# Kernel optimization log

Measured on AMD Instinct MI355X. Metric: run time of the kernel, lower is better.

The kernel has to match this reference:

```python
import jax, jax.numpy as jnp
import numpy as np

N = 100000   # nodes
E = 1600000  # edges (avg degree 16)
D = 128      # in_features == out_features (required by residual branch)


def setup_inputs() -> dict:
    key = jax.random.key(0)
    ks = jax.random.split(key, 8)
    return {
        "x": jax.random.normal(ks[0], (N, D), dtype=jnp.float32),
        "W": jax.random.normal(ks[1], (D, D), dtype=jnp.float32) * (1.0 / np.sqrt(D)),
        "b": jax.random.normal(ks[2], (D,), dtype=jnp.float32) * 0.01,
        "Wres": jax.random.normal(ks[3], (D, D), dtype=jnp.float32) * (1.0 / np.sqrt(D)),
        "bres": jax.random.normal(ks[4], (D,), dtype=jnp.float32) * 0.01,
        "edge_val": jax.random.uniform(ks[5], (E,), dtype=jnp.float32),
        "edge_row": jax.random.randint(ks[6], (E,), 0, N, dtype=jnp.int32),
        "edge_col": jax.random.randint(ks[7], (E,), 0, N, dtype=jnp.int32),
    }


def reference(x, W, b, Wres, bres, edge_val, edge_row, edge_col):
    # Dense projection: [N, D]
    h = x @ W + b
    # Sparse adjacency SpMM: out[i] = sum_{e: row[e]==i} val[e] * h[col[e]]
    msgs = edge_val[:, None] * h[edge_col]            # [E, D] gather
    agg = jax.ops.segment_sum(msgs, edge_row, num_segments=N)  # [N, D] scatter-add
    # Activation (relu), then residual Linear applied to post-activation tensor
    # (faithful to the torch code: x = act(x); x = x + residual(x)).
    a = jax.nn.relu(agg)
    out = a + (a @ Wres + bres)
    # dropout = 0.0 -> identity (eval mode)
    return out
```

## Files before the change

kernel.cpp:

```cpp
#include <hip/hip_runtime.h>
#include <hip/hip_bf16.h>

#define D 128
#define RCH 128
#define NCH 782
#define NCHP 1024
#define NB_S 500
#define CH_S 3200
#define OS2 800
#define CAP 3072
#define PB 128

typedef __attribute__((ext_vector_type(8))) short short8v;
typedef __attribute__((ext_vector_type(4))) float float4v;

__device__ inline ushort f2bf(float f) {
    __hip_bfloat16 h = __float2bfloat16(f);
    return __builtin_bit_cast(ushort, h);
}
__device__ inline float bf2f(ushort u) {
    return __builtin_bit_cast(float, (uint)u << 16);
}
__device__ inline ushort relu_bf(ushort u) { return (u & 0x8000u) ? (ushort)0 : u; }

__device__ inline void stage_wt_lds(char* smem, const ushort* __restrict__ Wt,
                                    int tid) {
#pragma unroll
    for (int i = 0; i < 8; ++i) {
        const int L = tid * 128 + i * 16;
        const int row = L >> 8;
        const int off = L & 255;
        *(short8v*)(smem + row * 256 + (off ^ ((row & 7) << 4))) =
            *(const short8v*)((const char*)Wt + L);
    }
}

__global__ __launch_bounds__(256) void k1_prep(const float* __restrict__ W,
                                               const float* __restrict__ Wres,
                                               ushort* __restrict__ Wt,
                                               ushort* __restrict__ Wtres) {
    const int flat = blockIdx.x * 256 + threadIdx.x;
    const float* src = (flat < 16384) ? W : Wres;
    ushort* dst = (flat < 16384) ? Wt : Wtres;
    const int f = flat & 16383;
    const int k = f >> 7, c = f & 127;
    dst[c * D + k] = f2bf(src[f]);
}

__global__ __launch_bounds__(256) void k3a_scatter(const float* __restrict__ ev,
                                                   const int* __restrict__ er,
                                                   const int* __restrict__ ec,
                                                   int* __restrict__ offs2,
                                                   int2* __restrict__ tmp, int E) {
    __shared__ int h[NCHP];
    __shared__ int sscan[256];
    const int b = blockIdx.x;
    const int t = threadIdx.x;
    const int start = b * CH_S;
    const int end = min(E, start + CH_S);
    const int nfull = (end - start) & ~3;

    for (int k = t; k < NCHP; k += 256) h[k] = 0;
    __syncthreads();

    for (int o = 4 * t; o < nfull; o += 1024) {
        const int4 r4 = *(const int4*)(er + start + o);
        atomicAdd(&h[r4.x >> 7], 1);
        atomicAdd(&h[r4.y >> 7], 1);
        atomicAdd(&h[r4.z >> 7], 1);
        atomicAdd(&h[r4.w >> 7], 1);
    }
    for (int o = nfull + t; o < end - start; o += 256)
        atomicAdd(&h[er[start + o] >> 7], 1);
    __syncthreads();

    const int a0 = h[4 * t], a1 = h[4 * t + 1];
    const int a2 = h[4 * t + 2], a3 = h[4 * t + 3];
    const int tsum = a0 + a1 + a2 + a3;
    sscan[t] = tsum;
    __syncthreads();
    for (int o = 1; o < 256; o <<= 1) {
        const int a = (t >= o) ? sscan[t - o] : 0;
        __syncthreads();
        sscan[t] += a;
        __syncthreads();
    }
    const int ex = start + sscan[t] - tsum;
    const int c0 = 4 * t;
    h[c0]     = ex;
    h[c0 + 1] = ex + a0;
    h[c0 + 2] = ex + a0 + a1;
    h[c0 + 3] = ex + a0 + a1 + a2;
    int* od = offs2 + (long)b * OS2;
#pragma unroll
    for (int i = 0; i < 4; ++i)
        if (c0 + i <= NCH) od[c0 + i] = h[c0 + i];
    __syncthreads();

    for (int o = 4 * t; o < nfull; o += 1024) {
        const int4 r4 = *(const int4*)(er + start + o);
        const int4 c4 = *(const int4*)(ec + start + o);
        const float4 v4 = *(const float4*)(ev + start + o);
        const int p0 = atomicAdd(&h[r4.x >> 7], 1);
        const int p1 = atomicAdd(&h[r4.y >> 7], 1);
        const int p2 = atomicAdd(&h[r4.z >> 7], 1);
        const int p3 = atomicAdd(&h[r4.w >> 7], 1);
        tmp[p0] = make_int2((c4.x << 7) | (r4.x & 127), __float_as_int(v4.x));
        tmp[p1] = make_int2((c4.y << 7) | (r4.y & 127), __float_as_int(v4.y));
        tmp[p2] = make_int2((c4.z << 7) | (r4.z & 127), __float_as_int(v4.z));
        tmp[p3] = make_int2((c4.w << 7) | (r4.w & 127), __float_as_int(v4.w));
    }
    for (int o = nfull + t; o < end - start; o += 256) {
        const int e = start + o;
        const int r = er[e];
        const int pos = atomicAdd(&h[r >> 7], 1);
        tmp[pos] = make_int2((ec[e] << 7) | (r & 127), __float_as_int(ev[e]));
    }
}

__global__ __launch_bounds__(256) void k3b_gemm0(const float* __restrict__ X,
                                                 const ushort* __restrict__ Wt,
                                                 const float* __restrict__ bias,
                                                 ushort* __restrict__ hb, int N) {
    __shared__ char smem[32768];
    const int lane = threadIdx.x & 63;
    const int w = threadIdx.x >> 6;
    const int l16 = lane & 15;
    const int lk = lane >> 4;

    stage_wt_lds(smem, Wt, threadIdx.x);
    __syncthreads();

    const int swz = (l16 & 7) << 4;

#pragma unroll
    for (int j = 0; j < 2; ++j) {
        const long wRow = (long)blockIdx.x * 128 + j * 64 + w * 16;

        short8v afrag[4];
        {
            long r = wRow + l16;
            if (r >= N) r = N - 1;
            const float* xp = X + r * D + lk * 8;
#pragma unroll
            for (int ks = 0; ks < 4; ++ks) {
                const float4 u0 = *(const float4*)(xp + ks * 32);
                const float4 u1 = *(const float4*)(xp + ks * 32 + 4);
                float f[8] = {u0.x, u0.y, u0.z, u0.w, u1.x, u1.y, u1.z, u1.w};
                short8v a;
#pragma unroll
                for (int i = 0; i < 8; ++i) a[i] = (short)f2bf(f[i]);
                afrag[ks] = a;
            }
        }

        float4v acc[8];
#pragma unroll
        for (int t = 0; t < 8; ++t) acc[t] = (float4v)(0.0f);

#pragma unroll
        for (int ks = 0; ks < 4; ++ks) {
#pragma unroll
            for (int t = 0; t < 8; ++t) {
                const int row = t * 16 + l16;
                const short8v bfrag = *(const short8v*)(
                    smem + row * 256 + ((ks * 64 + lk * 16) ^ swz));
                acc[t] = __builtin_amdgcn_mfma_f32_16x16x32_bf16(afrag[ks], bfrag,
                                                                 acc[t], 0, 0, 0);
            }
        }

#pragma unroll
        for (int t = 0; t < 8; ++t) {
            const int col = t * 16 + l16;
            const float bb = bias[col];
#pragma unroll
            for (int i = 0; i < 4; ++i) {
                const long row = wRow + lk * 4 + i;
                if (row < N) hb[row * D + col] = f2bf(acc[t][i] + bb);
            }
        }
    }
}

__global__ __launch_bounds__(256) void k4_sort(const int2* __restrict__ tmp,
                                               const int* __restrict__ offs2,
                                               int2* __restrict__ recs,
                                               int* __restrict__ rowptr) {
    __shared__ int2 buf[CAP];
    __shared__ int sb[256];
    __shared__ int hcnt[RCH];
    __shared__ int sc[RCH];
    __shared__ int cur[RCH];
    const int c = blockIdx.x;
    const int t = threadIdx.x;
    const int s = c * CAP;

    int segA = 0, cbA = 0, segB = 0, cbB = 0;
    if (t < NB_S / 2) {
        const int* oA = offs2 + (long)(2 * t) * OS2;
        const int* oB = offs2 + (long)(2 * t + 1) * OS2;
        segA = oA[c]; cbA = oA[c + 1] - segA;
        segB = oB[c]; cbB = oB[c + 1] - segB;
    }
    const int cb = cbA + cbB;

    sb[t] = cb;
    __syncthreads();
    for (int o = 1; o < 256; o <<= 1) {
        const int a = (t >= o) ? sb[t - o] : 0;
        __syncthreads();
        sb[t] += a;
        __syncthreads();
    }
    const int base = sb[t] - cb;
    const int cnt = min(sb[255], CAP);

    if (t < RCH) hcnt[t] = 0;
    __syncthreads();

    for (int i = 0; i < cbA; ++i) {
        const int p = base + i;
        if (p >= CAP) break;
        const int2 r = tmp[segA + i];
        buf[p] = r;
        atomicAdd(&hcnt[r.x & 127], 1);
    }
    for (int i = 0; i < cbB; ++i) {
        const int p = base + cbA + i;
        if (p >= CAP) break;
        const int2 r = tmp[segB + i];
        buf[p] = r;
        atomicAdd(&hcnt[r.x & 127], 1);
    }
    __syncthreads();

    if (t < RCH) sc[t] = hcnt[t];
    __syncthreads();
    for (int o = 1; o < RCH; o <<= 1) {
        const int a = (t < RCH && t >= o) ? sc[t - o] : 0;
        __syncthreads();
        if (t < RCH) sc[t] += a;
        __syncthreads();
    }
    if (t < RCH) {
        const int ex = s + sc[t] - hcnt[t];
        cur[t] = ex;
        rowptr[c * (RCH + 1) + t] = ex;
    }
    if (t == 0) rowptr[c * (RCH + 1) + RCH] = s + cnt;
    __syncthreads();

    for (int k = t; k < cnt; k += 256) {
        const int2 r = buf[k];
        const int pos = atomicAdd(&cur[r.x & 127], 1);
        recs[pos] = make_int2((r.x >> 7) << 8, r.y);
    }
}

#define GFMA2(accv, rr, gg)                                                   \
    accv.x = fmaf(__int_as_float((rr).y), bf2f((ushort)((gg)&0xffffu)), accv.x);\
    accv.y = fmaf(__int_as_float((rr).y), bf2f((ushort)((gg) >> 16)), accv.y);

__device__ inline void drain_row(const int2* __restrict__ recs,
                                 const char* __restrict__ hpc,
                                 int& j, int e, float2& acc) {
    for (; j + 8 <= e; j += 8) {
        const int2 r0 = recs[j],     r1 = recs[j + 1];
        const int2 r2 = recs[j + 2], r3 = recs[j + 3];
        const int2 r4 = recs[j + 4], r5 = recs[j + 5];
        const int2 r6 = recs[j + 6], r7 = recs[j + 7];
        const uint g0 = *(const uint*)(hpc + (uint)r0.x);
        const uint g1 = *(const uint*)(hpc + (uint)r1.x);
        const uint g2 = *(const uint*)(hpc + (uint)r2.x);
        const uint g3 = *(const uint*)(hpc + (uint)r3.x);
        const uint g4 = *(const uint*)(hpc + (uint)r4.x);
        const uint g5 = *(const uint*)(hpc + (uint)r5.x);
        const uint g6 = *(const uint*)(hpc + (uint)r6.x);
        const uint g7 = *(const uint*)(hpc + (uint)r7.x);
        GFMA2(acc, r0, g0) GFMA2(acc, r1, g1) GFMA2(acc, r2, g2) GFMA2(acc, r3, g3)
        GFMA2(acc, r4, g4) GFMA2(acc, r5, g5) GFMA2(acc, r6, g6) GFMA2(acc, r7, g7)
    }
    for (; j + 2 <= e; j += 2) {
        const int2 r0 = recs[j], r1 = recs[j + 1];
        const uint g0 = *(const uint*)(hpc + (uint)r0.x);
        const uint g1 = *(const uint*)(hpc + (uint)r1.x);
        GFMA2(acc, r0, g0) GFMA2(acc, r1, g1)
    }
    if (j < e) {
        const int2 r0 = recs[j];
        const uint g0 = *(const uint*)(hpc + (uint)r0.x);
        GFMA2(acc, r0, g0)
    }
}

__global__ __launch_bounds__(256) void k5_spmm(const ushort* __restrict__ hb,
                                               const int2* __restrict__ recs,
                                               const int* __restrict__ rowptr,
                                               ushort* __restrict__ aggb, int N) {
    const int pair = blockIdx.x * 4 + (threadIdx.x >> 6);
    const int lane = threadIdx.x & 63;
    const int rowA = pair * 2;
    if (rowA >= N) return;

    const int c = rowA >> 7;
    const int tr = rowA & 127;
    int rp = 0;
    if (lane < 3) rp = rowptr[c * (RCH + 1) + tr + lane];
    const int sA = __shfl(rp, 0);
    const int eA = __shfl(rp, 1);
    const int sB = eA;
    const int eB = __shfl(rp, 2);

    const char* hpc = (const char*)hb + lane * 4;
    float2 accA = make_float2(0.f, 0.f);
    float2 accB = make_float2(0.f, 0.f);

    int jA = sA, jB = sB;
    while (jA + 8 <= eA && jB + 8 <= eB) {
        const int2 a0 = recs[jA],     a1 = recs[jA + 1];
        const int2 a2 = recs[jA + 2], a3 = recs[jA + 3];
        const int2 a4 = recs[jA + 4], a5 = recs[jA + 5];
        const int2 a6 = recs[jA + 6], a7 = recs[jA + 7];
        const int2 b0 = recs[jB],     b1 = recs[jB + 1];
        const int2 b2 = recs[jB + 2], b3 = recs[jB + 3];
        const int2 b4 = recs[jB + 4], b5 = recs[jB + 5];
        const int2 b6 = recs[jB + 6], b7 = recs[jB + 7];
        const uint ga0 = *(const uint*)(hpc + (uint)a0.x);
        const uint ga1 = *(const uint*)(hpc + (uint)a1.x);
        const uint ga2 = *(const uint*)(hpc + (uint)a2.x);
        const uint ga3 = *(const uint*)(hpc + (uint)a3.x);
        const uint ga4 = *(const uint*)(hpc + (uint)a4.x);
        const uint ga5 = *(const uint*)(hpc + (uint)a5.x);
        const uint ga6 = *(const uint*)(hpc + (uint)a6.x);
        const uint ga7 = *(const uint*)(hpc + (uint)a7.x);
        const uint gb0 = *(const uint*)(hpc + (uint)b0.x);
        const uint gb1 = *(const uint*)(hpc + (uint)b1.x);
        const uint gb2 = *(const uint*)(hpc + (uint)b2.x);
        const uint gb3 = *(const uint*)(hpc + (uint)b3.x);
        const uint gb4 = *(const uint*)(hpc + (uint)b4.x);
        const uint gb5 = *(const uint*)(hpc + (uint)b5.x);
        const uint gb6 = *(const uint*)(hpc + (uint)b6.x);
        const uint gb7 = *(const uint*)(hpc + (uint)b7.x);
        GFMA2(accA, a0, ga0) GFMA2(accA, a1, ga1) GFMA2(accA, a2, ga2) GFMA2(accA, a3, ga3)
        GFMA2(accA, a4, ga4) GFMA2(accA, a5, ga5) GFMA2(accA, a6, ga6) GFMA2(accA, a7, ga7)
        GFMA2(accB, b0, gb0) GFMA2(accB, b1, gb1) GFMA2(accB, b2, gb2) GFMA2(accB, b3, gb3)
        GFMA2(accB, b4, gb4) GFMA2(accB, b5, gb5) GFMA2(accB, b6, gb6) GFMA2(accB, b7, gb7)
        jA += 8;
        jB += 8;
    }
    drain_row(recs, hpc, jA, eA, accA);
    drain_row(recs, hpc, jB, eB, accB);

    const uint pA = (uint)f2bf(accA.x) | ((uint)f2bf(accA.y) << 16);
    *(uint*)(aggb + (long)rowA * D + lane * 2) = pA;
    const uint pB = (uint)f2bf(accB.x) | ((uint)f2bf(accB.y) << 16);
    *(uint*)(aggb + (long)(rowA + 1) * D + lane * 2) = pB;
}

__global__ __launch_bounds__(256) void k6_gemm1(const ushort* __restrict__ Xb,
                                                const ushort* __restrict__ Wt,
                                                const float* __restrict__ bias,
                                                float* __restrict__ Y, int N) {
    __shared__ char smem[32768];
    const int lane = threadIdx.x & 63;
    const int w = threadIdx.x >> 6;
    const int l16 = lane & 15;
    const int lk = lane >> 4;
    const long wRow = (long)blockIdx.x * 64 + w * 16;

    short8v afrag[4];
    {
        long r = wRow + l16;
        if (r >= N) r = N - 1;
        const ushort* xp = Xb + r * D + lk * 8;
#pragma unroll
        for (int ks = 0; ks < 4; ++ks) {
            short8v a = *(const short8v*)(xp + ks * 32);
#pragma unroll
            for (int i = 0; i < 8; ++i) a[i] = (short)relu_bf((ushort)a[i]);
            afrag[ks] = a;
        }
    }

    stage_wt_lds(smem, Wt, threadIdx.x);
    __syncthreads();

    float4v acc[8];
#pragma unroll
    for (int t = 0; t < 8; ++t) acc[t] = (float4v)(0.0f);

    const int swz = (l16 & 7) << 4;
#pragma unroll
    for (int ks = 0; ks < 4; ++ks) {
#pragma unroll
        for (int t = 0; t < 8; ++t) {
            const int row = t * 16 + l16;
            const short8v bfrag = *(const short8v*)(
                smem + row * 256 + ((ks * 64 + lk * 16) ^ swz));
            acc[t] = __builtin_amdgcn_mfma_f32_16x16x32_bf16(afrag[ks], bfrag,
                                                             acc[t], 0, 0, 0);
        }
    }

#pragma unroll
    for (int t = 0; t < 8; ++t) {
        const int col = t * 16 + l16;
        const float bb = bias[col];
#pragma unroll
        for (int i = 0; i < 4; ++i) {
            const long row = wRow + lk * 4 + i;
            if (row < N) {
                const float a = bf2f(relu_bf(Xb[row * D + col]));
                Y[row * D + col] = a + acc[t][i] + bb;
            }
        }
    }
}

extern "C" void kernel_launch(void* const* d_in, const int* in_sizes, int n_in,
                              void* d_out, int out_size, void* d_ws, size_t ws_size,
                              hipStream_t stream) {
    const float* x    = (const float*)d_in[0];
    const float* W    = (const float*)d_in[1];
    const float* b    = (const float*)d_in[2];
    const float* Wres = (const float*)d_in[3];
    const float* bres = (const float*)d_in[4];
    const float* ev   = (const float*)d_in[5];
    const int*   er   = (const int*)d_in[6];
    const int*   ec   = (const int*)d_in[7];

    float* out = (float*)d_out;

    const int n = in_sizes[0] / D;
    const int e = in_sizes[5];

    char* ws = (char*)d_ws;
    size_t off_b = 0;
    auto alloc = [&](size_t bytes) {
        void* p = ws + off_b;
        off_b += (bytes + 511) & ~size_t(511);
        return p;
    };
    ushort* hb     = (ushort*)alloc((size_t)n * D * sizeof(ushort));
    int2*   recs   = (int2*)alloc((size_t)NCH * CAP * sizeof(int2));
    int*    rowptr = (int*)alloc((size_t)NCH * (RCH + 1) * sizeof(int));
    ushort* Wt     = (ushort*)alloc((size_t)D * D * sizeof(ushort));
    ushort* Wtres  = (ushort*)alloc((size_t)D * D * sizeof(ushort));
    const size_t overlay = off_b;
    int2*   tmp    = (int2*)alloc((size_t)NB_S * CH_S * sizeof(int2));
    int*    offs2  = (int*)alloc((size_t)NB_S * OS2 * sizeof(int));
    size_t aggb_end = overlay + (size_t)n * D * sizeof(ushort);
    if (aggb_end > off_b) off_b = aggb_end;
    ushort* aggb = (ushort*)(ws + overlay);
    (void)ws_size;

    k1_prep<<<PB, 256, 0, stream>>>(W, Wres, Wt, Wtres);

    k3a_scatter<<<NB_S, 256, 0, stream>>>(ev, er, ec, offs2, tmp, e);

    k3b_gemm0<<<(n + 127) / 128, 256, 0, stream>>>(x, Wt, b, hb, n);

    k4_sort<<<NCH, 256, 0, stream>>>(tmp, offs2, recs, rowptr);

    k5_spmm<<<(n / 2 + 3) / 4, 256, 0, stream>>>(hb, recs, rowptr, aggb, n);

    k6_gemm1<<<(n + 63) / 64, 256, 0, stream>>>(aggb, Wtres, bres, out, n);
}
```

Baseline: 162.4 us.

## Band-sort edges by source column and process four rows per wave in SpMM

The per-chunk counting sort now uses 2048 buckets keyed by destination row plus a high-bit band of the column byte offset, so each row's edges are ordered by column band. The aim is better L2/cache locality for the h gathers across waves running at the same time. The SpMM kernel also processes four rows per wavefront instead of two, with 32 independent gathers in flight to raise memory-level parallelism. The costs are a larger LDS footprint and a longer prefix scan in the sort, plus higher register pressure in the SpMM, which may lower occupancy.

```diff
diff --git a/kernel.cpp b/kernel.cpp
--- a/kernel.cpp
+++ b/kernel.cpp
@@ -10,6 +10,8 @@
 #define OS2 800
 #define CAP 3072
 #define PB 128
+#define NBKT 2048
+#define BANDSH 20
 
 typedef __attribute__((ext_vector_type(8))) short short8v;
 typedef __attribute__((ext_vector_type(4))) float float4v;
@@ -189,9 +191,8 @@
                                                int* __restrict__ rowptr) {
     __shared__ int2 buf[CAP];
     __shared__ int sb[256];
-    __shared__ int hcnt[RCH];
-    __shared__ int sc[RCH];
-    __shared__ int cur[RCH];
+    __shared__ int bcnt[NBKT];
+    __shared__ int bcur[NBKT];
     const int c = blockIdx.x;
     const int t = threadIdx.x;
     const int s = c * CAP;
@@ -206,6 +207,7 @@
     const int cb = cbA + cbB;
 
     sb[t] = cb;
+    for (int k = t; k < NBKT; k += 256) bcnt[k] = 0;
     __syncthreads();
     for (int o = 1; o < 256; o <<= 1) {
         const int a = (t >= o) ? sb[t - o] : 0;
@@ -216,44 +218,45 @@
     const int base = sb[t] - cb;
     const int cnt = min(sb[255], CAP);
 
-    if (t < RCH) hcnt[t] = 0;
-    __syncthreads();
-
     for (int i = 0; i < cbA; ++i) {
         const int p = base + i;
         if (p >= CAP) break;
         const int2 r = tmp[segA + i];
         buf[p] = r;
-        atomicAdd(&hcnt[r.x & 127], 1);
+        atomicAdd(&bcnt[((r.x & 127) << 4) | (r.x >> BANDSH)], 1);
     }
     for (int i = 0; i < cbB; ++i) {
         const int p = base + cbA + i;
         if (p >= CAP) break;
         const int2 r = tmp[segB + i];
         buf[p] = r;
-        atomicAdd(&hcnt[r.x & 127], 1);
-    }
-    __syncthreads();
-
-    if (t < RCH) sc[t] = hcnt[t];
-    __syncthreads();
-    for (int o = 1; o < RCH; o <<= 1) {
-        const int a = (t < RCH && t >= o) ? sc[t - o] : 0;
+        atomicAdd(&bcnt[((r.x & 127) << 4) | (r.x >> BANDSH)], 1);
+    }
+    __syncthreads();
+
+    int v[8];
+    int tsum = 0;
+#pragma unroll
+    for (int i = 0; i < 8; ++i) { v[i] = bcnt[8 * t + i]; tsum += v[i]; }
+    sb[t] = tsum;
+    __syncthreads();
+    for (int o = 1; o < 256; o <<= 1) {
+        const int a = (t >= o) ? sb[t - o] : 0;
         __syncthreads();
-        if (t < RCH) sc[t] += a;
+        sb[t] += a;
         __syncthreads();
     }
-    if (t < RCH) {
-        const int ex = s + sc[t] - hcnt[t];
-        cur[t] = ex;
-        rowptr[c * (RCH + 1) + t] = ex;
-    }
+    int run = s + sb[t] - tsum;
+#pragma unroll
+    for (int i = 0; i < 8; ++i) { bcur[8 * t + i] = run; run += v[i]; }
+    __syncthreads();
+    if (t < RCH) rowptr[c * (RCH + 1) + t] = bcur[t << 4];
     if (t == 0) rowptr[c * (RCH + 1) + RCH] = s + cnt;
     __syncthreads();
 
     for (int k = t; k < cnt; k += 256) {
         const int2 r = buf[k];
-        const int pos = atomicAdd(&cur[r.x & 127], 1);
+        const int pos = atomicAdd(&bcur[((r.x & 127) << 4) | (r.x >> BANDSH)], 1);
         recs[pos] = make_int2((r.x >> 7) << 8, r.y);
     }
 }
@@ -294,29 +297,10 @@
     }
 }
 
-__global__ __launch_bounds__(256) void k5_spmm(const ushort* __restrict__ hb,
-                                               const int2* __restrict__ recs,
-                                               const int* __restrict__ rowptr,
-                                               ushort* __restrict__ aggb, int N) {
-    const int pair = blockIdx.x * 4 + (threadIdx.x >> 6);
-    const int lane = threadIdx.x & 63;
-    const int rowA = pair * 2;
-    if (rowA >= N) return;
-
-    const int c = rowA >> 7;
-    const int tr = rowA & 127;
-    int rp = 0;
-    if (lane < 3) rp = rowptr[c * (RCH + 1) + tr + lane];
-    const int sA = __shfl(rp, 0);
-    const int eA = __shfl(rp, 1);
-    const int sB = eA;
-    const int eB = __shfl(rp, 2);
-
-    const char* hpc = (const char*)hb + lane * 4;
-    float2 accA = make_float2(0.f, 0.f);
-    float2 accB = make_float2(0.f, 0.f);
-
-    int jA = sA, jB = sB;
+__device__ inline void pair_loop(const int2* __restrict__ recs,
+                                 const char* __restrict__ hpc,
+                                 int& jA, int eA, int& jB, int eB,
+                                 float2& accA, float2& accB) {
     while (jA + 8 <= eA && jB + 8 <= eB) {
         const int2 a0 = recs[jA],     a1 = recs[jA + 1];
         const int2 a2 = recs[jA + 2], a3 = recs[jA + 3];
@@ -349,13 +333,68 @@
         jA += 8;
         jB += 8;
     }
-    drain_row(recs, hpc, jA, eA, accA);
-    drain_row(recs, hpc, jB, eB, accB);
-
-    const uint pA = (uint)f2bf(accA.x) | ((uint)f2bf(accA.y) << 16);
-    *(uint*)(aggb + (long)rowA * D + lane * 2) = pA;
-    const uint pB = (uint)f2bf(accB.x) | ((uint)f2bf(accB.y) << 16);
-    *(uint*)(aggb + (long)(rowA + 1) * D + lane * 2) = pB;
+}
+
+__global__ __launch_bounds__(256) void k5_spmm(const ushort* __restrict__ hb,
+                                               const int2* __restrict__ recs,
+                                               const int* __restrict__ rowptr,
+                                               ushort* __restrict__ aggb, int N) {
+    const int quad = blockIdx.x * 4 + (threadIdx.x >> 6);
+    const int lane = threadIdx.x & 63;
+    const int row0 = quad * 4;
+    if (row0 >= N) return;
+
+    const int c = row0 >> 7;
+    const int tr = row0 & 127;
+    int rp = 0;
+    if (lane < 5) rp = rowptr[c * (RCH + 1) + tr + lane];
+    int js[4], es[4];
+    js[0] = __shfl(rp, 0); es[0] = __shfl(rp, 1);
+    js[1] = es[0];         es[1] = __shfl(rp, 2);
+    js[2] = es[1];         es[2] = __shfl(rp, 3);
+    js[3] = es[2];         es[3] = __shfl(rp, 4);
+
+    const char* hpc = (const char*)hb + lane * 4;
+    float2 ac[4];
+#pragma unroll
+    for (int s = 0; s < 4; ++s) ac[s] = make_float2(0.f, 0.f);
+
+    while (js[0] + 8 <= es[0] && js[1] + 8 <= es[1] &&
+           js[2] + 8 <= es[2] && js[3] + 8 <= es[3]) {
+        int2 r[4][8];
+        uint g[4][8];
+#pragma unroll
+        for (int s = 0; s < 4; ++s) {
+#pragma unroll
+            for (int i = 0; i < 8; ++i) r[s][i] = recs[js[s] + i];
+        }
+#pragma unroll
+        for (int s = 0; s < 4; ++s) {
+#pragma unroll
+            for (int i = 0; i < 8; ++i)
+                g[s][i] = *(const uint*)(hpc + (uint)r[s][i].x);
+        }
+#pragma unroll
+        for (int s = 0; s < 4; ++s) {
+#pragma unroll
+            for (int i = 0; i < 8; ++i) { GFMA2(ac[s], r[s][i], g[s][i]) }
+            js[s] += 8;
+        }
+    }
+
+    pair_loop(recs, hpc, js[0], es[0], js[1], es[1], ac[0], ac[1]);
+    pair_loop(recs, hpc, js[2], es[2], js[3], es[3], ac[2], ac[3]);
+
+    drain_row(recs, hpc, js[0], es[0], ac[0]);
+    drain_row(recs, hpc, js[1], es[1], ac[1]);
+    drain_row(recs, hpc, js[2], es[2], ac[2]);
+    drain_row(recs, hpc, js[3], es[3], ac[3]);
+
+#pragma unroll
+    for (int s = 0; s < 4; ++s) {
+        const uint p = (uint)f2bf(ac[s].x) | ((uint)f2bf(ac[s].y) << 16);
+        *(uint*)(aggb + (long)(row0 + s) * D + lane * 2) = p;
+    }
 }
 
 __global__ __launch_bounds__(256) void k6_gemm1(const ushort* __restrict__ Xb,
@@ -463,7 +502,7 @@
 
     k4_sort<<<NCH, 256, 0, stream>>>(tmp, offs2, recs, rowptr);
 
-    k5_spmm<<<(n / 2 + 3) / 4, 256, 0, stream>>>(hb, recs, rowptr, aggb, n);
+    k5_spmm<<<(n / 4 + 3) / 4, 256, 0, stream>>>(hb, recs, rowptr, aggb, n);
 
     k6_gemm1<<<(n + 63) / 64, 256, 0, stream>>>(aggb, Wtres, bres, out, n);
 }
```

Result: slower. 175.7 us (+8.2%).

## Merge independent kernels into heterogeneous launches to cut launch count

Applied to the files above, without the earlier changes.

Folds the weight-transpose prep blocks into the edge scatter kernel and the bucket sort blocks into the first GEMM kernel, selecting the role by block index. This takes the launch count from six to four and lets independent work share one grid. The GEMM part now handles 64 rows per block instead of 128, so twice as many blocks each restage the weights into LDS. The sort's shared buffers are carved out of the GEMM's 32 KB shared array, so both roles get the same LDS footprint.

```diff
diff --git a/kernel.cpp b/kernel.cpp
--- a/kernel.cpp
+++ b/kernel.cpp
@@ -10,6 +10,7 @@
 #define OS2 800
 #define CAP 3072
 #define PB 128
+#define GB64 1563
 
 typedef __attribute__((ext_vector_type(8))) short short8v;
 typedef __attribute__((ext_vector_type(4))) float float4v;
@@ -35,25 +36,25 @@
     }
 }
 
-__global__ __launch_bounds__(256) void k1_prep(const float* __restrict__ W,
-                                               const float* __restrict__ Wres,
-                                               ushort* __restrict__ Wt,
-                                               ushort* __restrict__ Wtres) {
-    const int flat = blockIdx.x * 256 + threadIdx.x;
-    const float* src = (flat < 16384) ? W : Wres;
-    ushort* dst = (flat < 16384) ? Wt : Wtres;
-    const int f = flat & 16383;
-    const int k = f >> 7, c = f & 127;
-    dst[c * D + k] = f2bf(src[f]);
-}
-
-__global__ __launch_bounds__(256) void k3a_scatter(const float* __restrict__ ev,
-                                                   const int* __restrict__ er,
-                                                   const int* __restrict__ ec,
-                                                   int* __restrict__ offs2,
-                                                   int2* __restrict__ tmp, int E) {
+__global__ __launch_bounds__(256) void kA_scatter_prep(
+    const float* __restrict__ W, const float* __restrict__ Wres,
+    ushort* __restrict__ Wt, ushort* __restrict__ Wtres,
+    const float* __restrict__ ev, const int* __restrict__ er,
+    const int* __restrict__ ec, int* __restrict__ offs2,
+    int2* __restrict__ tmp, int E) {
     __shared__ int h[NCHP];
     __shared__ int sscan[256];
+
+    if (blockIdx.x >= NB_S) {
+        const int flat = (blockIdx.x - NB_S) * 256 + threadIdx.x;
+        const float* src = (flat < 16384) ? W : Wres;
+        ushort* dst = (flat < 16384) ? Wt : Wtres;
+        const int f = flat & 16383;
+        const int k = f >> 7, c = f & 127;
+        dst[c * D + k] = f2bf(src[f]);
+        return;
+    }
+
     const int b = blockIdx.x;
     const int t = threadIdx.x;
     const int start = b * CH_S;
@@ -118,143 +119,139 @@
     }
 }
 
-__global__ __launch_bounds__(256) void k3b_gemm0(const float* __restrict__ X,
-                                                 const ushort* __restrict__ Wt,
-                                                 const float* __restrict__ bias,
-                                                 ushort* __restrict__ hb, int N) {
+__global__ __launch_bounds__(256) void kB_sort_gemm(
+    const int2* __restrict__ tmp, const int* __restrict__ offs2,
+    int2* __restrict__ recs, int* __restrict__ rowptr,
+    const float* __restrict__ X, const ushort* __restrict__ Wt,
+    const float* __restrict__ bias, ushort* __restrict__ hb, int N) {
     __shared__ char smem[32768];
-    const int lane = threadIdx.x & 63;
-    const int w = threadIdx.x >> 6;
+    const int t = threadIdx.x;
+
+    if (blockIdx.x < NCH) {
+        int2* buf = (int2*)smem;
+        int*  sb  = (int*)(smem + 24576);
+        int*  hcnt = (int*)(smem + 25600);
+        int*  sc  = (int*)(smem + 26112);
+        int*  cur = (int*)(smem + 26624);
+        const int c = blockIdx.x;
+        const int s = c * CAP;
+
+        int segA = 0, cbA = 0, segB = 0, cbB = 0;
+        if (t < NB_S / 2) {
+            const int* oA = offs2 + (long)(2 * t) * OS2;
+            const int* oB = offs2 + (long)(2 * t + 1) * OS2;
+            segA = oA[c]; cbA = oA[c + 1] - segA;
+            segB = oB[c]; cbB = oB[c + 1] - segB;
+        }
+        const int cb = cbA + cbB;
+
+        sb[t] = cb;
+        __syncthreads();
+        for (int o = 1; o < 256; o <<= 1) {
+            const int a = (t >= o) ? sb[t - o] : 0;
+            __syncthreads();
+            sb[t] += a;
+            __syncthreads();
+        }
+        const int base = sb[t] - cb;
+        const int cnt = min(sb[255], CAP);
+
+        if (t < RCH) hcnt[t] = 0;
+        __syncthreads();
+
+        for (int i = 0; i < cbA; ++i) {
+            const int p = base + i;
+            if (p >= CAP) break;
+            const int2 r = tmp[segA + i];
+            buf[p] = r;
+            atomicAdd(&hcnt[r.x & 127], 1);
+        }
+        for (int i = 0; i < cbB; ++i) {
+            const int p = base + cbA + i;
+            if (p >= CAP) break;
+            const int2 r = tmp[segB + i];
+            buf[p] = r;
+            atomicAdd(&hcnt[r.x & 127], 1);
+        }
+        __syncthreads();
+
+        if (t < RCH) sc[t] = hcnt[t];
+        __syncthreads();
+        for (int o = 1; o < RCH; o <<= 1) {
+            const int a = (t < RCH && t >= o) ? sc[t - o] : 0;
+            __syncthreads();
+            if (t < RCH) sc[t] += a;
+            __syncthreads();
+        }
+        if (t < RCH) {
+            const int ex = s + sc[t] - hcnt[t];
+            cur[t] = ex;
+            rowptr[c * (RCH + 1) + t] = ex;
+        }
+        if (t == 0) rowptr[c * (RCH + 1) + RCH] = s + cnt;
+        __syncthreads();
+
+        for (int k = t; k < cnt; k += 256) {
+            const int2 r = buf[k];
+            const int pos = atomicAdd(&cur[r.x & 127], 1);
+            recs[pos] = make_int2((r.x >> 7) << 8, r.y);
+        }
+        return;
+    }
+
+    const int g = blockIdx.x - NCH;
+    const int lane = t & 63;
+    const int w = t >> 6;
     const int l16 = lane & 15;
     const int lk = lane >> 4;
-
-    stage_wt_lds(smem, Wt, threadIdx.x);
-    __syncthreads();
+    const long wRow = (long)g * 64 + w * 16;
+
+    short8v afrag[4];
+    {
+        long r = wRow + l16;
+        if (r >= N) r = N - 1;
+        const float* xp = X + r * D + lk * 8;
+#pragma unroll
+        for (int ks = 0; ks < 4; ++ks) {
+            const float4 u0 = *(const float4*)(xp + ks * 32);
+            const float4 u1 = *(const float4*)(xp + ks * 32 + 4);
+            float f[8] = {u0.x, u0.y, u0.z, u0.w, u1.x, u1.y, u1.z, u1.w};
+            short8v a;
+#pragma unroll
+            for (int i = 0; i < 8; ++i) a[i] = (short)f2bf(f[i]);
+            afrag[ks] = a;
+        }
+    }
+
+    stage_wt_lds(smem, Wt, t);
+    __syncthreads();
+
+    float4v acc[8];
+#pragma unroll
+    for (int q = 0; q < 8; ++q) acc[q] = (float4v)(0.0f);
 
     const int swz = (l16 & 7) << 4;
-
-#pragma unroll
-    for (int j = 0; j < 2; ++j) {
-        const long wRow = (long)blockIdx.x * 128 + j * 64 + w * 16;
-
-        short8v afrag[4];
-        {
-            long r = wRow + l16;
-            if (r >= N) r = N - 1;
-            const float* xp = X + r * D + lk * 8;
-#pragma unroll
-            for (int ks = 0; ks < 4; ++ks) {
-                const float4 u0 = *(const float4*)(xp + ks * 32);
-                const float4 u1 = *(const float4*)(xp + ks * 32 + 4);
-                float f[8] = {u0.x, u0.y, u0.z, u0.w, u1.x, u1.y, u1.z, u1.w};
-                short8v a;
-#pragma unroll
-                for (int i = 0; i < 8; ++i) a[i] = (short)f2bf(f[i]);
-                afrag[ks] = a;
-            }
-        }
-
-        float4v acc[8];
-#pragma unroll
-        for (int t = 0; t < 8; ++t) acc[t] = (float4v)(0.0f);
-
-#pragma unroll
-        for (int ks = 0; ks < 4; ++ks) {
-#pragma unroll
-            for (int t = 0; t < 8; ++t) {
-                const int row = t * 16 + l16;
-                const short8v bfrag = *(const short8v*)(
-                    smem + row * 256 + ((ks * 64 + lk * 16) ^ swz));
-                acc[t] = __builtin_amdgcn_mfma_f32_16x16x32_bf16(afrag[ks], bfrag,
-                                                                 acc[t], 0, 0, 0);
-            }
-        }
-
-#pragma unroll
-        for (int t = 0; t < 8; ++t) {
-            const int col = t * 16 + l16;
-            const float bb = bias[col];
-#pragma unroll
-            for (int i = 0; i < 4; ++i) {
-                const long row = wRow + lk * 4 + i;
-                if (row < N) hb[row * D + col] = f2bf(acc[t][i] + bb);
-            }
-        }
-    }
-}
-
-__global__ __launch_bounds__(256) void k4_sort(const int2* __restrict__ tmp,
-                                               const int* __restrict__ offs2,
-                                               int2* __restrict__ recs,
-                                               int* __restrict__ rowptr) {
-    __shared__ int2 buf[CAP];
-    __shared__ int sb[256];
-    __shared__ int hcnt[RCH];
-    __shared__ int sc[RCH];
-    __shared__ int cur[RCH];
-    const int c = blockIdx.x;
-    const int t = threadIdx.x;
-    const int s = c * CAP;
-
-    int segA = 0, cbA = 0, segB = 0, cbB = 0;
-    if (t < NB_S / 2) {
-        const int* oA = offs2 + (long)(2 * t) * OS2;
-        const int* oB = offs2 + (long)(2 * t + 1) * OS2;
-        segA = oA[c]; cbA = oA[c + 1] - segA;
-        segB = oB[c]; cbB = oB[c + 1] - segB;
-    }
-    const int cb = cbA + cbB;
-
-    sb[t] = cb;
-    __syncthreads();
-    for (int o = 1; o < 256; o <<= 1) {
-        const int a = (t >= o) ? sb[t - o] : 0;
-        __syncthreads();
-        sb[t] += a;
-        __syncthreads();
-    }
-    const int base = sb[t] - cb;
-    const int cnt = min(sb[255], CAP);
-
-    if (t < RCH) hcnt[t] = 0;
-    __syncthreads();
-
-    for (int i = 0; i < cbA; ++i) {
-        const int p = base + i;
-        if (p >= CAP) break;
-        const int2 r = tmp[segA + i];
-        buf[p] = r;
-        atomicAdd(&hcnt[r.x & 127], 1);
-    }
-    for (int i = 0; i < cbB; ++i) {
-        const int p = base + cbA + i;
-        if (p >= CAP) break;
-        const int2 r = tmp[segB + i];
-        buf[p] = r;
-        atomicAdd(&hcnt[r.x & 127], 1);
-    }
-    __syncthreads();
-
-    if (t < RCH) sc[t] = hcnt[t];
-    __syncthreads();
-    for (int o = 1; o < RCH; o <<= 1) {
-        const int a = (t < RCH && t >= o) ? sc[t - o] : 0;
-        __syncthreads();
-        if (t < RCH) sc[t] += a;
-        __syncthreads();
-    }
-    if (t < RCH) {
-        const int ex = s + sc[t] - hcnt[t];
-        cur[t] = ex;
-        rowptr[c * (RCH + 1) + t] = ex;
-    }
-    if (t == 0) rowptr[c * (RCH + 1) + RCH] = s + cnt;
-    __syncthreads();
-
-    for (int k = t; k < cnt; k += 256) {
-        const int2 r = buf[k];
-        const int pos = atomicAdd(&cur[r.x & 127], 1);
-        recs[pos] = make_int2((r.x >> 7) << 8, r.y);
+#pragma unroll
+    for (int ks = 0; ks < 4; ++ks) {
+#pragma unroll
+        for (int q = 0; q < 8; ++q) {
+            const int row = q * 16 + l16;
+            const short8v bfrag = *(const short8v*)(
+                smem + row * 256 + ((ks * 64 + lk * 16) ^ swz));
+            acc[q] = __builtin_amdgcn_mfma_f32_16x16x32_bf16(afrag[ks], bfrag,
+                                                             acc[q], 0, 0, 0);
+        }
+    }
+
+#pragma unroll
+    for (int q = 0; q < 8; ++q) {
+        const int col = q * 16 + l16;
+        const float bb = bias[col];
+#pragma unroll
+        for (int i = 0; i < 4; ++i) {
+            const long row = wRow + lk * 4 + i;
+            if (row < N) hb[row * D + col] = f2bf(acc[q][i] + bb);
+        }
     }
 }
 
@@ -388,31 +385,31 @@
 
     float4v acc[8];
 #pragma unroll
-    for (int t = 0; t < 8; ++t) acc[t] = (float4v)(0.0f);
+    for (int q = 0; q < 8; ++q) acc[q] = (float4v)(0.0f);
 
     const int swz = (l16 & 7) << 4;
 #pragma unroll
     for (int ks = 0; ks < 4; ++ks) {
 #pragma unroll
-        for (int t = 0; t < 8; ++t) {
-            const int row = t * 16 + l16;
+        for (int q = 0; q < 8; ++q) {
+            const int row = q * 16 + l16;
             const short8v bfrag = *(const short8v*)(
                 smem + row * 256 + ((ks * 64 + lk * 16) ^ swz));
-            acc[t] = __builtin_amdgcn_mfma_f32_16x16x32_bf16(afrag[ks], bfrag,
-                                                             acc[t], 0, 0, 0);
-        }
-    }
-
-#pragma unroll
-    for (int t = 0; t < 8; ++t) {
-        const int col = t * 16 + l16;
+            acc[q] = __builtin_amdgcn_mfma_f32_16x16x32_bf16(afrag[ks], bfrag,
+                                                             acc[q], 0, 0, 0);
+        }
+    }
+
+#pragma unroll
+    for (int q = 0; q < 8; ++q) {
+        const int col = q * 16 + l16;
         const float bb = bias[col];
 #pragma unroll
         for (int i = 0; i < 4; ++i) {
             const long row = wRow + lk * 4 + i;
             if (row < N) {
                 const float a = bf2f(relu_bf(Xb[row * D + col]));
-                Y[row * D + col] = a + acc[t][i] + bb;
+                Y[row * D + col] = a + acc[q][i] + bb;
             }
         }
     }
@@ -455,13 +452,11 @@
     ushort* aggb = (ushort*)(ws + overlay);
     (void)ws_size;
 
-    k1_prep<<<PB, 256, 0, stream>>>(W, Wres, Wt, Wtres);
-
-    k3a_scatter<<<NB_S, 256, 0, stream>>>(ev, er, ec, offs2, tmp, e);
-
-    k3b_gemm0<<<(n + 127) / 128, 256, 0, stream>>>(x, Wt, b, hb, n);
-
-    k4_sort<<<NCH, 256, 0, stream>>>(tmp, offs2, recs, rowptr);
+    kA_scatter_prep<<<NB_S + PB, 256, 0, stream>>>(W, Wres, Wt, Wtres,
+                                                   ev, er, ec, offs2, tmp, e);
+
+    kB_sort_gemm<<<NCH + GB64, 256, 0, stream>>>(tmp, offs2, recs, rowptr,
+                                                 x, Wt, b, hb, n);
 
     k5_spmm<<<(n / 2 + 3) / 4, 256, 0, stream>>>(hb, recs, rowptr, aggb, n);
 
```

New measurement: 153.0 us. -5.8%, faster.
